# Kernel optimization log

Hardware: AMD Instinct MI355X
Metric: run time of the kernel (lower is better)

Reference implementation:

```python
import jax, jax.numpy as jnp
import numpy as np

N = 32768   # 'a' nodes
K = 8       # incoming edges per node (regular graph)
K2 = K // 2
E = N * K   # edges, stored as reverse pairs (2i, 2i+1)
D = 300     # hid_dim
H = 4       # attention heads
DEPTH = 3


def _build_graph():
    i = np.arange(N)
    src = np.empty(E, np.int64)
    mail = np.empty((N, K), np.int64)
    for d in range(1, K2 + 1):
        base = 2 * (i * K2 + (d - 1))
        src[base] = i                 # edge i -> (i+d)%N
        src[base + 1] = (i + d) % N   # reverse edge (i+d)%N -> i
        # incoming edges of node v: ((v-d)->v) and ((v+d)->v)
        mail[:, 2 * (d - 1)] = 2 * (((i - d) % N) * K2 + (d - 1))
        mail[:, 2 * (d - 1) + 1] = 2 * (i * K2 + (d - 1)) + 1
    return src, mail


def setup_inputs() -> dict:
    key = jax.random.key(0)
    ks = jax.random.split(key, 12)
    s = 1.0 / np.sqrt(D)
    src, mail = _build_graph()
    return {
        'f': jax.random.normal(ks[0], (N, D), jnp.float32),
        'x': jax.random.normal(ks[1], (E, D), jnp.float32),
        'mail_idx': jnp.asarray(mail),
        'src_idx': jnp.asarray(src),
        'Wq': jax.random.normal(ks[2], (D, D), jnp.float32) * s,
        'bq': jnp.zeros((D,), jnp.float32),
        'Wk': jax.random.normal(ks[3], (D, D), jnp.float32) * s,
        'bk': jnp.zeros((D,), jnp.float32),
        'Wv': jax.random.normal(ks[4], (D, D), jnp.float32) * s,
        'bv': jnp.zeros((D,), jnp.float32),
        'Wo': jax.random.normal(ks[5], (D, D), jnp.float32) * s,
        'bo': jnp.zeros((D,), jnp.float32),
        'Wmp': jax.random.normal(ks[6], (DEPTH - 1, D, D), jnp.float32) * s,
        'bmp': jnp.zeros((DEPTH - 1, D), jnp.float32),
        'Wlast': jax.random.normal(ks[7], (3 * D, D), jnp.float32) * s,
        'blast': jnp.zeros((D,), jnp.float32),
    }


def _mha(q_in, k_in, v_in, Wq, bq, Wk, bk, Wv, bv, Wo, bo):
    # q_in: [N,1,D], k_in/v_in: [N,K,D]  (per-node neighborhood attention)
    dk = D // H
    q = (q_in @ Wq + bq).reshape(N, 1, H, dk).transpose(0, 2, 1, 3)
    k = (k_in @ Wk + bk).reshape(N, -1, H, dk).transpose(0, 2, 1, 3)
    v = (v_in @ Wv + bv).reshape(N, -1, H, dk).transpose(0, 2, 1, 3)
    scores = jnp.einsum('nhqd,nhkd->nhqk', q, k) / jnp.sqrt(jnp.float32(dk))
    p = jax.nn.softmax(scores, axis=-1)
    o = jnp.einsum('nhqk,nhkd->nhqd', p, v).transpose(0, 2, 1, 3).reshape(N, 1, D)
    return o @ Wo + bo


def reference(f, x, mail_idx, src_idx, Wq, bq, Wk, bk, Wv, bv, Wo, bo,
              Wmp, bmp, Wlast, blast):
    rev = jnp.arange(E) ^ 1  # reverse_edge: swap within consecutive pairs
    f_h = f              # init_node: f_h = f.clone()
    h = x                # init_edge: h = x.clone()
    for i in range(DEPTH - 1):
        mail = h[mail_idx]                    # copy_e mailbox [N,K,D]
        feat = f_h[:, None, :]                # [N,1,D]
        # add_attn: attn(feat, mail, mail + feat)
        f_h = _mha(feat, mail, mail + feat,
                   Wq, bq, Wk, bk, Wv, bv, Wo, bo)[:, 0, :]
        rev_h = h[rev]                        # paired reverse-edge feature
        m = f_h[src_idx] - rev_h              # del_reverse_message
        h = jax.nn.relu(x + m @ Wmp[i] + bmp[i])  # update_edge
    # final node update: Linear(cat([sum(mailbox h), f_h, f]))
    mail_sum = jnp.sum(h[mail_idx], axis=1)   # [N,D]
    f_final = jnp.concatenate([mail_sum, f_h, f], axis=1) @ Wlast + blast
    return f_final
```

## Files before the change

kernel.cpp:

```cpp
#include <hip/hip_runtime.h>

typedef unsigned short u16;
typedef unsigned int u32;
typedef __bf16 bf16x8 __attribute__((ext_vector_type(8)));
typedef float f32x4 __attribute__((ext_vector_type(4)));

#define N_NODES 32768
#define E_EDGES 262144
#define BQ_U16 26240
#define S75 0.11547005383792515f

__device__ __forceinline__ float b2f(u16 u) {
    union { u32 u; float f; } x; x.u = ((u32)u) << 16; return x.f;
}
__device__ __forceinline__ u16 f2b(float f) {
    union { float f; u32 u; } x; x.f = f;
    u32 r = x.u + 0x7FFF + ((x.u >> 16) & 1);
    return (u16)(r >> 16);
}

#define GLOAD16(g, l) \
    __builtin_amdgcn_global_load_lds((const __attribute__((address_space(1))) u32*)(g), \
                                     (__attribute__((address_space(3))) u32*)(l), 16, 0, 0)

__global__ void convT_k(const float* __restrict__ src, int R, int C,
                        u16* __restrict__ dst, int KP_, long total) {
    long id = (long)blockIdx.x * blockDim.x + threadIdx.x;
    if (id >= total) return;
    int n = (int)(id / KP_), k = (int)(id % KP_);
    dst[id] = (k < R && n < C) ? f2b(src[(long)k * C + n]) : (u16)0;
}

__global__ void convTq_k(const float* __restrict__ src, u16* __restrict__ dst) {
    int id = blockIdx.x * 256 + threadIdx.x;
    if (id >= 4 * BQ_U16) return;
    int q = id / BQ_U16, rem = id % BQ_U16;
    int r = rem / 328, c = rem % 328;
    int n = q * 80 + r;
    dst[id] = (c < 300 && n < 300) ? f2b(src[(long)c * 300 + n]) : (u16)0;
}

__global__ void wqkq_k(const float* __restrict__ Wq, const float* __restrict__ Wk,
                       u16* __restrict__ dst) {
    int id = blockIdx.x * 256 + threadIdx.x;
    if (id >= 16 * BQ_U16) return;
    int q = id / BQ_U16, rem = id % BQ_U16;
    int r = rem / 328, c = rem % 328;
    int h = q >> 2;
    int cc = (q & 3) * 80 + r;
    float acc = 0.f;
    if (c < 300 && cc < 300) {
        const float* wq = Wq + (long)c * 300 + 75 * h;
        const float* wk = Wk + (long)cc * 300 + 75 * h;
        for (int d = 0; d < 75; ++d) acc += wq[d] * wk[d];
        acc *= S75;
    }
    dst[id] = f2b(acc);
}

__global__ void bqk_k(const float* __restrict__ bq, const float* __restrict__ Wk,
                      float* __restrict__ dst) {
    int n = blockIdx.x * 256 + threadIdx.x;
    if (n >= 1280) return;
    int h = n / 320, cc = n % 320;
    float acc = 0.f;
    if (cc < 300) {
        const float* b = bq + 75 * h;
        const float* wk = Wk + (long)cc * 300 + 75 * h;
        for (int d = 0; d < 75; ++d) acc += b[d] * wk[d];
        acc *= S75;
    }
    dst[n] = acc;
}

__global__ void ucatp_k(const float* __restrict__ Wv, const float* __restrict__ Wo,
                        u16* __restrict__ dst) {
    long id = (long)blockIdx.x * 256 + threadIdx.x;
    if (id >= 4L * 5 * BQ_U16) return;
    int q = (int)(id / (5 * BQ_U16));
    int rem = (int)(id % (5 * BQ_U16));
    int ph = rem / BQ_U16;
    int rem2 = rem % BQ_U16;
    int r = rem2 / 328, c = rem2 % 328;
    int n = q * 80 + r;
    float acc = 0.f;
    if (n < 300 && c < 320) {
        if (ph < 4) {
            int a = c;
            if (a < 300) {
                const float* wv = Wv + (long)a * 300 + 75 * ph;
                const float* wo = Wo + (long)(75 * ph) * 300 + n;
                for (int d = 0; d < 75; ++d) acc += wv[d] * wo[(long)d * 300];
            }
        } else {
            int a = c;
            if (a < 300) {
                const float* wv = Wv + (long)a * 300;
                const float* wo = Wo + n;
                for (int d = 0; d < 300; ++d) acc += wv[d] * wo[(long)d * 300];
            }
        }
    }
    dst[id] = f2b(acc);
}

__global__ void bvo_k(const float* __restrict__ bv, const float* __restrict__ Wo,
                      const float* __restrict__ bo, float* __restrict__ dst) {
    int n = blockIdx.x * 256 + threadIdx.x;
    if (n >= 320) return;
    float acc = 0.f;
    if (n < 300) {
        for (int d = 0; d < 300; ++d) acc += bv[d] * Wo[(long)d * 300 + n];
        acc += bo[n];
    }
    dst[n] = acc;
}

__global__ void padconv_k(const float* __restrict__ src, int C,
                          u16* __restrict__ dst, int CP,
                          u16* __restrict__ dst2, int CP2, long total) {
    long id = (long)blockIdx.x * blockDim.x + threadIdx.x;
    if (id >= total) return;
    int cw = CP >> 3;
    long row = id / cw;
    int c8 = (int)(id % cw) * 8;
    u32 w[4];
    #pragma unroll
    for (int p = 0; p < 4; ++p) {
        int c0 = c8 + 2 * p, c1 = c0 + 1;
        u16 lo = (c0 < C) ? f2b(src[row * C + c0]) : (u16)0;
        u16 hi = (c1 < C) ? f2b(src[row * C + c1]) : (u16)0;
        w[p] = (u32)lo | ((u32)hi << 16);
    }
    u32* d = (u32*)(dst + row * CP + c8);
    d[0] = w[0]; d[1] = w[1]; d[2] = w[2]; d[3] = w[3];
    if (dst2) {
        u32* d2 = (u32*)(dst2 + row * CP2 + c8);
        d2[0] = w[0]; d2[1] = w[1]; d2[2] = w[2]; d2[3] = w[3];
    }
}

__global__ void featcopy_k(const u16* __restrict__ src, u16* __restrict__ dst) {
    long id = (long)blockIdx.x * 256 + threadIdx.x;
    if (id >= (long)N_NODES * 40) return;
    long row = id / 40;
    int c8 = (int)(id % 40) * 8;
    *(uint4*)&dst[row * 1600 + 1280 + c8] = *(const uint4*)&src[row * 320 + c8];
}


#define GEMM16_SHARED \
    __shared__ __attribute__((aligned(16))) u16 Bs[3328 * 8];      \
    __shared__ __attribute__((aligned(16))) u16 dumpB[512];        \
    __shared__ __attribute__((aligned(16))) u16 As3[3][512 * 32];

#define GEMM16_PRE(QBITS, LDA) \
    const int tid = threadIdx.x; \
    const int w = tid >> 6, lane = tid & 63; \
    const int tl = lane & 15, thi = lane >> 4; \
    const int bid = blockIdx.x; \
    const int gid = (bid & 7) * ((int)gridDim.x >> 3) + (bid >> 3); \
    const long m0 = (long)(gid >> (QBITS)) * 512; \
    const int q = gid & ((1 << (QBITS)) - 1); \
    const int n0 = q * 80; \
    const int w_u = __builtin_amdgcn_readfirstlane(w); \
    const u16* Bsrc = Bswz + q * BQ_U16; \
     \
    _Pragma("unroll") \
    for (int i = 0; i < 3; ++i) \
        GLOAD16(Bsrc + (long)(i * 1024 + tid) * 8, &Bs[(i * 1024 + w_u * 64) * 8]); \
    { \
        int t = 3072 + tid; \
        int ts = t < 3280 ? t : 3279; \
        u16* bdst = (w_u < 4) ? &Bs[(3072 + w_u * 64) * 8] : dumpB; \
        GLOAD16(Bsrc + (long)ts * 8, bdst); \
    } \
    __builtin_amdgcn_sched_barrier(0); \
     \
    const int rr = lane >> 2;                  \
    const int gsrc = (lane & 3) ^ (rr & 3);    \
    const u16* pA0 = A + (m0 + w * 32 + rr) * (long)(LDA) + gsrc * 8; \
    const u16* pA1 = pA0 + 16L * (LDA); \
    u16* awbase = &As3[0][0];

#define ASTAGE16(KB) { \
    u16* d_ = &As3[(KB) % 3][w_u * 1024]; \
    GLOAD16(pA0 + (KB) * 32, d_); \
    GLOAD16(pA1 + (KB) * 32, d_ + 512); }

#define TCOMP16(KB) { \
    const u16* aw_ = &As3[(KB) % 3][w * 1024]; \
    bf16x8 a0_ = *(const bf16x8*)&aw_[tl * 32 + (thi ^ (tl & 3)) * 8]; \
    bf16x8 a1_ = *(const bf16x8*)&aw_[512 + tl * 32 + (thi ^ (tl & 3)) * 8]; \
    __builtin_amdgcn_s_setprio(1); \
    _Pragma("unroll") for (int fc = 0; fc < 5; ++fc) { \
        bf16x8 bb_ = *(const bf16x8*)&Bs[tl * 328 + thi * 8 + fc * 5248 + (KB) * 32]; \
        acc[0][fc] = __builtin_amdgcn_mfma_f32_16x16x32_bf16(bb_, a0_, acc[0][fc], 0, 0, 0); \
        acc[1][fc] = __builtin_amdgcn_mfma_f32_16x16x32_bf16(bb_, a1_, acc[1][fc], 0, 0, 0); } \
    __builtin_amdgcn_s_setprio(0); }

#define GEMM16_LOOP \
    ASTAGE16(0); ASTAGE16(1); ASTAGE16(2); \
    f32x4 acc[2][5]; \
    _Pragma("unroll") for (int i = 0; i < 2; ++i) \
        _Pragma("unroll") for (int j = 0; j < 5; ++j) acc[i][j] = (f32x4)(0.f); \
    asm volatile("s_waitcnt vmcnt(6)" ::: "memory");    \
    __builtin_amdgcn_s_barrier();                       \
    __builtin_amdgcn_sched_barrier(0); \
     \
    _Pragma("unroll") \
    for (int KB = 0; KB < 10; ++KB) { \
        if (KB <= 7)      { asm volatile("s_waitcnt vmcnt(4)" ::: "memory"); } \
        else if (KB == 8) { asm volatile("s_waitcnt vmcnt(2)" ::: "memory"); } \
        else              { asm volatile("s_waitcnt vmcnt(0)" ::: "memory"); } \
        __builtin_amdgcn_sched_barrier(0); \
        TCOMP16(KB); \
        asm volatile("s_waitcnt lgkmcnt(0)" ::: "memory");   \
        __builtin_amdgcn_sched_barrier(0); \
        if (KB + 3 < 10) ASTAGE16(KB + 3); \
    } \
    (void)awbase;

template<int QBITS, int OSTR>
__global__ __launch_bounds__(1024, 4) void ngemm16_k(
    const u16* __restrict__ A, const u16* __restrict__ Bswz,
    const float* __restrict__ bias, u16* __restrict__ outB)
{
    GEMM16_SHARED
    GEMM16_PRE(QBITS, 320)
    GEMM16_LOOP

    #pragma unroll
    for (int fr = 0; fr < 2; ++fr) {
        const long row = m0 + w * 32 + fr * 16 + tl;
        #pragma unroll
        for (int fc = 0; fc < 5; ++fc) {
            const int c0 = n0 + fc * 16 + thi * 4;
            f32x4 v = acc[fr][fc];
            if (bias) {
                const float4 bs = *(const float4*)&bias[c0];
                v[0] += bs.x; v[1] += bs.y; v[2] += bs.z; v[3] += bs.w;
            }
            uint2 p;
            p.x = (u32)f2b(v[0]) | ((u32)f2b(v[1]) << 16);
            p.y = (u32)f2b(v[2]) | ((u32)f2b(v[3]) << 16);
            *(uint2*)&outB[row * (long)OSTR + c0] = p;
        }
    }
}

__global__ __launch_bounds__(1024, 4) void hgemm16_k(
    const u16* __restrict__ A , const u16* __restrict__ Bswz ,
    const u16* __restrict__ FG, const u16* __restrict__ hx,
    const int* __restrict__ srcidx, const float* __restrict__ bias,
    u16* __restrict__ outB)
{
    GEMM16_SHARED
    GEMM16_PRE(2, 320)
    GEMM16_LOOP

    #pragma unroll
    for (int fr = 0; fr < 2; ++fr) {
        const long row = m0 + w * 32 + fr * 16 + tl;
        const int srow = srcidx[row];
        #pragma unroll
        for (int fc = 0; fc < 5; ++fc) {
            const int c0 = n0 + fc * 16 + thi * 4;
            float o0 = __shfl_xor(acc[fr][fc][0], 1, 64);
            float o1 = __shfl_xor(acc[fr][fc][1], 1, 64);
            float o2 = __shfl_xor(acc[fr][fc][2], 1, 64);
            float o3 = __shfl_xor(acc[fr][fc][3], 1, 64);
            const ushort4 fg = *(const ushort4*)&FG[(long)srow * 320 + c0];
            const ushort4 xv = *(const ushort4*)&hx[row * 320 + c0];
            float v0 = b2f(fg.x) + b2f(xv.x) - o0;
            float v1 = b2f(fg.y) + b2f(xv.y) - o1;
            float v2 = b2f(fg.z) + b2f(xv.z) - o2;
            float v3 = b2f(fg.w) + b2f(xv.w) - o3;
            if (c0 < 300) {
                const float4 bs = *(const float4*)&bias[c0];
                v0 += bs.x; v1 += bs.y; v2 += bs.z; v3 += bs.w;
            }
            v0 = fmaxf(v0, 0.f); v1 = fmaxf(v1, 0.f);
            v2 = fmaxf(v2, 0.f); v3 = fmaxf(v3, 0.f);
            uint2 p;
            p.x = (u32)f2b(v0) | ((u32)f2b(v1) << 16);
            p.y = (u32)f2b(v2) | ((u32)f2b(v3) << 16);
            *(uint2*)&outB[row * 320 + c0] = p;
        }
    }
}

#define TCOMP(KB, APTR) do { \
    bf16x8 av_[2], bb_[5]; \
    _Pragma("unroll") for (int fr = 0; fr < 2; ++fr) \
        av_[fr] = *(const bf16x8*)&(APTR)[ar0 + fr * 512]; \
    _Pragma("unroll") for (int fc = 0; fc < 5; ++fc) \
        bb_[fc] = *(const bf16x8*)&Bsw[br0 + fc * 5248 + (KB) * 32]; \
    __builtin_amdgcn_s_setprio(1); \
    _Pragma("unroll") for (int fr = 0; fr < 2; ++fr) \
        _Pragma("unroll") for (int fc = 0; fc < 5; ++fc) \
            acc[fr][fc] = __builtin_amdgcn_mfma_f32_16x16x32_bf16(bb_[fc], av_[fr], acc[fr][fc], 0, 0, 0); \
    __builtin_amdgcn_s_setprio(0); \
} while (0)

__global__ __launch_bounds__(256, 2) void wgemm_k(
    const u16* __restrict__ A , const u16* __restrict__ Bp,
    const float* __restrict__ bias, u16* __restrict__ outB)
{
    __shared__ __attribute__((aligned(16))) u16 Bsw[80 * 328];
    __shared__ __attribute__((aligned(16))) u16 As3[3][128 * 32];
    const int tid = threadIdx.x;
    const int wf = tid >> 6, lane = tid & 63;
    const int tl = lane & 15, thi = lane >> 4;
    const int bid = blockIdx.x;
    const int gid = (bid & 7) * ((int)gridDim.x >> 3) + (bid >> 3);
    const long m0 = (long)(gid >> 2) * 128;
    const int q = gid & 3;
    const int n0 = q * 80;
    const int wf_u = __builtin_amdgcn_readfirstlane(wf);
    const u16* BsrcQ = Bp + (long)q * (5 * BQ_U16);

    const int r1 = tid >> 2;
    const int g1 = (tid & 3) ^ ((r1 >> 1) & 3);
    const u16* gA0 = A + (m0 + r1) * 1600L + g1 * 8;
    const u16* gA1 = A + (m0 + 64 + r1) * 1600L + g1 * 8;

    f32x4 acc[2][5];
    #pragma unroll
    for (int i = 0; i < 2; ++i)
        #pragma unroll
        for (int j = 0; j < 5; ++j) acc[i][j] = (f32x4)(0.f);
    const int ar0 = (wf * 32 + tl) * 32 + (thi ^ ((tl >> 1) & 3)) * 8;
    const int br0 = tl * 328 + thi * 8;

    #pragma unroll
    for (int ph = 0; ph < 5; ++ph) {
        if (ph) __syncthreads();
        const u16* Bsrc = BsrcQ + ph * BQ_U16;
        #pragma unroll
        for (int i = 0; i < 13; ++i) {
            int t = i * 256 + tid;
            if (t < 3280)
                GLOAD16(Bsrc + (long)t * 8, &Bsw[(i * 256 + wf_u * 64) * 8]);
        }
        const long ko = (long)ph * 320;

#define WSTAGE(KB) { \
    GLOAD16(gA0 + ko + (KB) * 32, &As3[(KB) % 3][wf_u * 512]); \
    GLOAD16(gA1 + ko + (KB) * 32, &As3[(KB) % 3][2048 + wf_u * 512]); }

        WSTAGE(0); WSTAGE(1);

#define WSTEP(KB, VN) { \
    asm volatile("s_waitcnt vmcnt(" #VN ")" ::: "memory"); \
    __builtin_amdgcn_s_barrier(); \
    __builtin_amdgcn_sched_barrier(0); \
    if ((KB) + 2 < 10) WSTAGE((KB) + 2); \
    TCOMP(KB, (&As3[(KB) % 3][0])); }

        WSTEP(0, 2) WSTEP(1, 2) WSTEP(2, 2) WSTEP(3, 2) WSTEP(4, 2)
        WSTEP(5, 2) WSTEP(6, 2) WSTEP(7, 2) WSTEP(8, 2) WSTEP(9, 0)
#undef WSTEP
#undef WSTAGE
    }

    #pragma unroll
    for (int fr = 0; fr < 2; ++fr) {
        const long row = m0 + wf * 32 + fr * 16 + tl;
        #pragma unroll
        for (int fc = 0; fc < 5; ++fc) {
            const int c0 = n0 + fc * 16 + thi * 4;
            f32x4 v = acc[fr][fc];
            const float4 bs = *(const float4*)&bias[c0];
            v[0] += bs.x; v[1] += bs.y; v[2] += bs.z; v[3] += bs.w;
            uint2 p;
            p.x = (u32)f2b(v[0]) | ((u32)f2b(v[1]) << 16);
            p.y = (u32)f2b(v[2]) | ((u32)f2b(v[3]) << 16);
            *(uint2*)&outB[row * 320 + c0] = p;
        }
    }
}

__global__ __launch_bounds__(256) void attn2_k(
    const u16* __restrict__ qg, const u16* __restrict__ hcur,
    const int* __restrict__ mail, u16* __restrict__ wideA)
{
    const int tid = threadIdx.x;
    const long n = (long)blockIdx.x * 4 + (tid >> 6);
    const int lane = tid & 63;
    const bool act = lane < 40;
    const int ll = act ? lane : 39;

    int idx[8];
    #pragma unroll
    for (int j = 0; j < 8; ++j) idx[j] = mail[n * 8 + j];
    uint4 hr[8];
    #pragma unroll
    for (int j = 0; j < 8; ++j)
        hr[j] = *(const uint4*)&hcur[(long)idx[j] * 320 + ll * 8];
    uint4 qv[4];
    #pragma unroll
    for (int h = 0; h < 4; ++h)
        qv[h] = *(const uint4*)&qg[n * 1280 + h * 320 + ll * 8];
    if (!act) {
        #pragma unroll
        for (int j = 0; j < 8; ++j) hr[j] = make_uint4(0, 0, 0, 0);
    }

    float qf[4][8];
    #pragma unroll
    for (int h = 0; h < 4; ++h) {
        const u32 w[4] = {qv[h].x, qv[h].y, qv[h].z, qv[h].w};
        #pragma unroll
        for (int p = 0; p < 4; ++p) {
            qf[h][2 * p]     = b2f((u16)(w[p] & 0xFFFF));
            qf[h][2 * p + 1] = b2f((u16)(w[p] >> 16));
        }
    }

    float s[4][8];
    #pragma unroll
    for (int j = 0; j < 8; ++j) {
        float hf[8];
        const u32 w[4] = {hr[j].x, hr[j].y, hr[j].z, hr[j].w};
        #pragma unroll
        for (int p = 0; p < 4; ++p) {
            hf[2 * p]     = b2f((u16)(w[p] & 0xFFFF));
            hf[2 * p + 1] = b2f((u16)(w[p] >> 16));
        }
        #pragma unroll
        for (int h = 0; h < 4; ++h) {
            float d = 0.f;
            #pragma unroll
            for (int m = 0; m < 8; ++m) d += qf[h][m] * hf[m];
            d += __shfl_xor(d, 32, 64);
            d += __shfl_xor(d, 16, 64);
            d += __shfl_xor(d, 8, 64);
            d += __shfl_xor(d, 4, 64);
            d += __shfl_xor(d, 2, 64);
            d += __shfl_xor(d, 1, 64);
            s[h][j] = d;
        }
    }

    float p_[4][8];
    #pragma unroll
    for (int h = 0; h < 4; ++h) {
        float mx = s[h][0];
        #pragma unroll
        for (int j = 1; j < 8; ++j) mx = fmaxf(mx, s[h][j]);
        float sum = 0.f;
        #pragma unroll
        for (int j = 0; j < 8; ++j) { p_[h][j] = __expf(s[h][j] - mx); sum += p_[h][j]; }
        const float inv = 1.f / sum;
        #pragma unroll
        for (int j = 0; j < 8; ++j) p_[h][j] *= inv;
    }

    float y[4][8];
    #pragma unroll
    for (int h = 0; h < 4; ++h)
        #pragma unroll
        for (int m = 0; m < 8; ++m) y[h][m] = 0.f;
    #pragma unroll
    for (int j = 0; j < 8; ++j) {
        float hf[8];
        const u32 w[4] = {hr[j].x, hr[j].y, hr[j].z, hr[j].w};
        #pragma unroll
        for (int p = 0; p < 4; ++p) {
            hf[2 * p]     = b2f((u16)(w[p] & 0xFFFF));
            hf[2 * p + 1] = b2f((u16)(w[p] >> 16));
        }
        #pragma unroll
        for (int h = 0; h < 4; ++h)
            #pragma unroll
            for (int m = 0; m < 8; ++m) y[h][m] += p_[h][j] * hf[m];
    }
    if (act) {
        #pragma unroll
        for (int h = 0; h < 4; ++h) {
            uint4 o;
            o.x = (u32)f2b(y[h][0]) | ((u32)f2b(y[h][1]) << 16);
            o.y = (u32)f2b(y[h][2]) | ((u32)f2b(y[h][3]) << 16);
            o.z = (u32)f2b(y[h][4]) | ((u32)f2b(y[h][5]) << 16);
            o.w = (u32)f2b(y[h][6]) | ((u32)f2b(y[h][7]) << 16);
            *(uint4*)&wideA[n * 1600 + h * 320 + lane * 8] = o;
        }
    }
}

#define LOADB(bq, kt1) { const long ko_ = (long)(kt1) << 6; \
    _Pragma("unroll") for (int fc = 0; fc < 5; ++fc) \
      _Pragma("unroll") for (int ks = 0; ks < 2; ++ks) \
        bq[fc][ks] = *(const bf16x8*)(gBw + (long)fc * 16 * KP + ko_ + ks * 32); }

#define READA(lkt) { \
    _Pragma("unroll") for (int fr = 0; fr < 4; ++fr) \
      _Pragma("unroll") for (int ks = 0; ks < 2; ++ks) \
        a[fr][ks] = *(const bf16x8*)&As[(fr * 16 + tl) * 320 + ((((lkt) * 8 + ks * 4 + thi) ^ sx) * 8)]; }

#define DOMFMA(bq) { _Pragma("unroll") for (int fr = 0; fr < 4; ++fr) \
    _Pragma("unroll") for (int fc = 0; fc < 5; ++fc) \
      _Pragma("unroll") for (int ks = 0; ks < 2; ++ks) \
        acc[fr][fc] = __builtin_amdgcn_mfma_f32_16x16x32_bf16(bq[fc][ks], a[fr][ks], acc[fr][fc], 0, 0, 0); }

template<int KP>
__global__ __launch_bounds__(256, 2) void gemm_k(
    const u16* __restrict__ A,
    const u16* __restrict__ BT,
    const float* __restrict__ bias,
    float* __restrict__ outF, int ostride, int ocols)
{
    __shared__ u16 As[64 * 320];
    const int tid = threadIdx.x;
    const int w = tid >> 6, lane = tid & 63;
    const int tl = lane & 15, thi = lane >> 4;
    const int sx = tl & 7;
    const long m0 = (long)blockIdx.x * 64;
    const int w_u = __builtin_amdgcn_readfirstlane(w);

    const u16* gBw = BT + ((long)(w * 80 + tl)) * KP + thi * 8;

    f32x4 acc[4][5];
    #pragma unroll
    for (int i = 0; i < 4; ++i)
        #pragma unroll
        for (int j = 0; j < 5; ++j) acc[i][j] = (f32x4)(0.f);

    constexpr int NCH = KP / 320;
    constexpr int NST = KP >> 6;
    bf16x8 bA[5][2], bB[5][2], a[4][2];

    #pragma unroll
    for (int kb = 0; kb < NCH; ++kb) {
        if (kb) __syncthreads();
        #pragma unroll
        for (int i = 0; i < 10; ++i) {
            const int c = i * 256 + w_u * 64 + lane;
            const int r = c / 40, s = c - r * 40;
            GLOAD16(A + (m0 + r) * (long)KP + kb * 320 + ((s ^ (r & 7)) * 8),
                    &As[(i * 256 + w_u * 64) * 8]);
        }
        if (kb == 0) LOADB(bA, 0);
        __syncthreads();
        #pragma unroll
        for (int lkt = 0; lkt < 5; ++lkt) {
            const int kt = kb * 5 + lkt;
            if (kt + 1 < NST) {
                if (kt & 1) { LOADB(bA, kt + 1); } else { LOADB(bB, kt + 1); }
            }
            READA(lkt);
            if (kt & 1) { DOMFMA(bB); } else { DOMFMA(bA); }
        }
    }

    #pragma unroll
    for (int fr = 0; fr < 4; ++fr) {
        const long row = m0 + fr * 16 + tl;
        #pragma unroll
        for (int fc = 0; fc < 5; ++fc) {
            const int c0 = w * 80 + fc * 16 + thi * 4;
            f32x4 v = acc[fr][fc];
            if (bias && c0 < 300) {
                const float4 bs = *(const float4*)&bias[c0];
                v[0] += bs.x; v[1] += bs.y; v[2] += bs.z; v[3] += bs.w;
            }
            if (c0 < ocols)
                *(float4*)&outF[row * (long)ostride + c0] = make_float4(v[0], v[1], v[2], v[3]);
        }
    }
}

__global__ __launch_bounds__(256) void concat_k(
    const u16* __restrict__ hb, const u16* __restrict__ fhb,
    const float* __restrict__ f, const int* __restrict__ mail,
    u16* __restrict__ Acat)
{
    const long n = blockIdx.x;
    int m[8];
    #pragma unroll
    for (int j = 0; j < 8; ++j) m[j] = mail[n * 8 + j];
    for (int c = threadIdx.x; c < 960; c += 256) {
        float v;
        if (c < 300) {
            float s = 0.f;
            #pragma unroll
            for (int j = 0; j < 8; ++j) s += b2f(hb[(long)m[j] * 320 + c]);
            v = s;
        } else if (c < 600) v = b2f(fhb[n * 320 + (c - 300)]);
        else if (c < 900) v = f[n * 300 + (c - 600)];
        else v = 0.f;
        Acat[n * 960 + c] = f2b(v);
    }
}

extern "C" void kernel_launch(void* const* d_in, const int* in_sizes, int n_in,
                              void* d_out, int out_size, void* d_ws, size_t ws_size,
                              hipStream_t stream)
{
    const int N = N_NODES, E = E_EDGES;
    const float* f    = (const float*)d_in[0];
    const float* x    = (const float*)d_in[1];
    const int*   mail = (const int*)d_in[2];
    const int*   srcx = (const int*)d_in[3];
    const float* Wq = (const float*)d_in[4];   const float* bq = (const float*)d_in[5];
    const float* Wk = (const float*)d_in[6];
    const float* Wv = (const float*)d_in[8];   const float* bv = (const float*)d_in[9];
    const float* Wo = (const float*)d_in[10];  const float* bo = (const float*)d_in[11];
    const float* Wmp = (const float*)d_in[12]; const float* bmp = (const float*)d_in[13];
    const float* Wlast = (const float*)d_in[14]; const float* blast = (const float*)d_in[15];
    float* out = (float*)d_out;

    char* ws = (char*)d_ws;
    size_t off = 0;
    auto alloc = [&](size_t b) -> void* {
        void* p = ws + off; off += (b + 255) & ~(size_t)255; return p;
    };
    u16* hb    = (u16*)alloc((size_t)E * 320 * 2);
    u16* hb2   = (u16*)alloc((size_t)E * 320 * 2);
    u16* qgb   = (u16*)alloc((size_t)N * 1280 * 2);
    u16* wideA = (u16*)alloc((size_t)N * 1600 * 2);
    u16* fhb   = (u16*)alloc((size_t)N * 320 * 2);
    u16* FGb   = (u16*)alloc((size_t)N * 320 * 2);
    u16* Acat  = (u16*)alloc((size_t)N * 960 * 2);
    u16* WqkS  = (u16*)alloc((size_t)16 * BQ_U16 * 2);
    u16* Wm0S  = (u16*)alloc((size_t)4 * BQ_U16 * 2);
    u16* Wm1S  = (u16*)alloc((size_t)4 * BQ_U16 * 2);
    u16* UcatP = (u16*)alloc((size_t)4 * 5 * BQ_U16 * 2);
    u16* WcatB = (u16*)alloc((size_t)960 * 320 * 2);
    float* bqkF = (float*)alloc(1280 * 4);
    float* bvoF = (float*)alloc(320 * 4);

    {
        wqkq_k<<<(16 * BQ_U16 + 255) / 256, 256, 0, stream>>>(Wq, Wk, WqkS);
        bqk_k<<<5, 256, 0, stream>>>(bq, Wk, bqkF);
        ucatp_k<<<(int)((4L * 5 * BQ_U16 + 255) / 256), 256, 0, stream>>>(Wv, Wo, UcatP);
        bvo_k<<<2, 256, 0, stream>>>(bv, Wo, bo, bvoF);
        int blks = (4 * BQ_U16 + 255) / 256;
        convTq_k<<<blks, 256, 0, stream>>>(Wmp, Wm0S);
        convTq_k<<<blks, 256, 0, stream>>>(Wmp + 90000, Wm1S);
        long totc = (long)320 * 960;
        convT_k<<<(int)((totc + 255) / 256), 256, 0, stream>>>(Wlast, 900, 300, WcatB, 960, totc);
    }
    {
        long totE = (long)E * 40;
        padconv_k<<<(int)((totE + 255) / 256), 256, 0, stream>>>(x, 300, hb, 320, nullptr, 0, totE);
        long totN = (long)N * 40;
        padconv_k<<<(int)((totN + 255) / 256), 256, 0, stream>>>(f, 300, fhb, 320, wideA + 1280, 1600, totN);
    }

    const int GQG = (N / 512) * 16;
    const int GFG = (N / 512) * 4;
    const int GNW = (N / 128) * 4;
    const int GEH = (E / 512) * 4;

    for (int it = 0; it < 2; ++it) {
        const float* bmpi = bmp + it * 300;
        const u16* WmS = it ? Wm1S : Wm0S;
        const u16* hcur = it ? hb2 : hb;
        u16* hnxt = it ? hb : hb2;
        ngemm16_k<4, 1280><<<GQG, 1024, 0, stream>>>(fhb, WqkS, bqkF, qgb);
        attn2_k<<<N / 4, 256, 0, stream>>>(qgb, hcur, mail, wideA);
        wgemm_k<<<GNW, 256, 0, stream>>>(wideA, UcatP, bvoF, fhb);
        featcopy_k<<<(int)(((long)N * 40 + 255) / 256), 256, 0, stream>>>(fhb, wideA);
        ngemm16_k<2, 320><<<GFG, 1024, 0, stream>>>(fhb, WmS, nullptr, FGb);
        hgemm16_k<<<GEH, 1024, 0, stream>>>(hcur, WmS, FGb, hb, srcx, bmpi, hnxt);
    }

    concat_k<<<N, 256, 0, stream>>>(hb, fhb, f, mail, Acat);
    gemm_k<960><<<N / 64, 256, 0, stream>>>(Acat, WcatB, blast, out, 300, 300);
}
```

Measured before the change: 1.337 ms.

## Restructure bf16 GEMMs to keep A tile resident and loop over N-panels

Replaces the 1024-thread, 512-row GEMM kernels (one 80-column B panel per block, triple-buffered A streaming) with 512-thread kernels that load a 128-row A tile into LDS once and iterate over all output column panels, restaging B per panel. This cuts repeated reads of A across column panels and the grid-level panel decomposition. The cost is serialized B staging with __syncthreads and no overlap between B loads and compute. The bias is also pre-padded to 320 entries so the epilogue drops its bounds check.

```diff
diff --git a/kernel.cpp b/kernel.cpp
--- a/kernel.cpp
+++ b/kernel.cpp
@@ -116,6 +116,13 @@
     dst[n] = acc;
 }
 
+__global__ void padb_k(const float* __restrict__ bmp, float* __restrict__ dst) {
+    int id = blockIdx.x * 256 + threadIdx.x;
+    if (id >= 640) return;
+    int it = id / 320, c = id % 320;
+    dst[id] = (c < 300) ? bmp[it * 300 + c] : 0.f;
+}
+
 __global__ void padconv_k(const float* __restrict__ src, int C,
                           u16* __restrict__ dst, int CP,
                           u16* __restrict__ dst2, int CP2, long total) {
@@ -149,94 +156,73 @@
 }
 
 
-#define GEMM16_SHARED \
-    __shared__ __attribute__((aligned(16))) u16 Bs[3328 * 8];      \
-    __shared__ __attribute__((aligned(16))) u16 dumpB[512];        \
-    __shared__ __attribute__((aligned(16))) u16 As3[3][512 * 32];
-
-#define GEMM16_PRE(QBITS, LDA) \
+#define PG_SHARED \
+    __shared__ __attribute__((aligned(16))) u16 Al[128 * 328]; \
+    __shared__ __attribute__((aligned(16))) u16 Bs[80 * 328];
+
+#define PG_PRE \
     const int tid = threadIdx.x; \
     const int w = tid >> 6, lane = tid & 63; \
     const int tl = lane & 15, thi = lane >> 4; \
-    const int bid = blockIdx.x; \
-    const int gid = (bid & 7) * ((int)gridDim.x >> 3) + (bid >> 3); \
-    const long m0 = (long)(gid >> (QBITS)) * 512; \
-    const int q = gid & ((1 << (QBITS)) - 1); \
-    const int n0 = q * 80; \
+    const long m0 = (long)blockIdx.x * 128; \
     const int w_u = __builtin_amdgcn_readfirstlane(w); \
-    const u16* Bsrc = Bswz + q * BQ_U16; \
      \
     _Pragma("unroll") \
-    for (int i = 0; i < 3; ++i) \
-        GLOAD16(Bsrc + (long)(i * 1024 + tid) * 8, &Bs[(i * 1024 + w_u * 64) * 8]); \
-    { \
-        int t = 3072 + tid; \
-        int ts = t < 3280 ? t : 3279; \
-        u16* bdst = (w_u < 4) ? &Bs[(3072 + w_u * 64) * 8] : dumpB; \
-        GLOAD16(Bsrc + (long)ts * 8, bdst); \
+    for (int j = 0; j < 10; ++j) { \
+        int slot = j * 512 + tid; \
+        int r = slot / 41, s = slot % 41; \
+        GLOAD16(A + (m0 + r) * 320L + (s < 40 ? s : 39) * 8, \
+                &Al[(j * 512 + w_u * 64) * 8]); \
     } \
-    __builtin_amdgcn_sched_barrier(0); \
-     \
-    const int rr = lane >> 2;                  \
-    const int gsrc = (lane & 3) ^ (rr & 3);    \
-    const u16* pA0 = A + (m0 + w * 32 + rr) * (long)(LDA) + gsrc * 8; \
-    const u16* pA1 = pA0 + 16L * (LDA); \
-    u16* awbase = &As3[0][0];
-
-#define ASTAGE16(KB) { \
-    u16* d_ = &As3[(KB) % 3][w_u * 1024]; \
-    GLOAD16(pA0 + (KB) * 32, d_); \
-    GLOAD16(pA1 + (KB) * 32, d_ + 512); }
-
-#define TCOMP16(KB) { \
-    const u16* aw_ = &As3[(KB) % 3][w * 1024]; \
-    bf16x8 a0_ = *(const bf16x8*)&aw_[tl * 32 + (thi ^ (tl & 3)) * 8]; \
-    bf16x8 a1_ = *(const bf16x8*)&aw_[512 + tl * 32 + (thi ^ (tl & 3)) * 8]; \
-    __builtin_amdgcn_s_setprio(1); \
-    _Pragma("unroll") for (int fc = 0; fc < 5; ++fc) { \
-        bf16x8 bb_ = *(const bf16x8*)&Bs[tl * 328 + thi * 8 + fc * 5248 + (KB) * 32]; \
-        acc[0][fc] = __builtin_amdgcn_mfma_f32_16x16x32_bf16(bb_, a0_, acc[0][fc], 0, 0, 0); \
-        acc[1][fc] = __builtin_amdgcn_mfma_f32_16x16x32_bf16(bb_, a1_, acc[1][fc], 0, 0, 0); } \
-    __builtin_amdgcn_s_setprio(0); }
-
-#define GEMM16_LOOP \
-    ASTAGE16(0); ASTAGE16(1); ASTAGE16(2); \
-    f32x4 acc[2][5]; \
-    _Pragma("unroll") for (int i = 0; i < 2; ++i) \
-        _Pragma("unroll") for (int j = 0; j < 5; ++j) acc[i][j] = (f32x4)(0.f); \
-    asm volatile("s_waitcnt vmcnt(6)" ::: "memory");    \
-    __builtin_amdgcn_s_barrier();                       \
-    __builtin_amdgcn_sched_barrier(0); \
-     \
+    if (tid < 128) { \
+        int slot = 5120 + tid; \
+        int r = slot / 41, s = slot % 41; \
+        GLOAD16(A + (m0 + r) * 320L + (s < 40 ? s : 39) * 8, \
+                &Al[(5120 + w_u * 64) * 8]); \
+    }
+
+#define PG_STAGEB(QQ) { \
+    const u16* Bsrc_ = Bq + (QQ) * BQ_U16; \
+    _Pragma("unroll") \
+    for (int j = 0; j < 7; ++j) { \
+        int t = j * 512 + tid; \
+        if (t < 3280) \
+            GLOAD16(Bsrc_ + (long)t * 8, &Bs[(j * 512 + w_u * 64) * 8]); \
+    } }
+
+#define PG_COMPUTE \
+    f32x4 acc[5]; \
+    _Pragma("unroll") for (int fc = 0; fc < 5; ++fc) acc[fc] = (f32x4)(0.f); \
     _Pragma("unroll") \
     for (int KB = 0; KB < 10; ++KB) { \
-        if (KB <= 7)      { asm volatile("s_waitcnt vmcnt(4)" ::: "memory"); } \
-        else if (KB == 8) { asm volatile("s_waitcnt vmcnt(2)" ::: "memory"); } \
-        else              { asm volatile("s_waitcnt vmcnt(0)" ::: "memory"); } \
-        __builtin_amdgcn_sched_barrier(0); \
-        TCOMP16(KB); \
-        asm volatile("s_waitcnt lgkmcnt(0)" ::: "memory");   \
-        __builtin_amdgcn_sched_barrier(0); \
-        if (KB + 3 < 10) ASTAGE16(KB + 3); \
-    } \
-    (void)awbase;
-
-template<int QBITS, int OSTR>
-__global__ __launch_bounds__(1024, 4) void ngemm16_k(
-    const u16* __restrict__ A, const u16* __restrict__ Bswz,
+        bf16x8 a_ = *(const bf16x8*)&Al[(w * 16 + tl) * 328 + thi * 8 + KB * 32]; \
+        __builtin_amdgcn_s_setprio(1); \
+        _Pragma("unroll") for (int fc = 0; fc < 5; ++fc) { \
+            bf16x8 bb_ = *(const bf16x8*)&Bs[(fc * 16 + tl) * 328 + thi * 8 + KB * 32]; \
+            acc[fc] = __builtin_amdgcn_mfma_f32_16x16x32_bf16(bb_, a_, acc[fc], 0, 0, 0); \
+        } \
+        __builtin_amdgcn_s_setprio(0); \
+    }
+
+template<int NPH, int OSTR>
+__global__ __launch_bounds__(512, 2) void pgemm_k(
+    const u16* __restrict__ A, const u16* __restrict__ Bq,
     const float* __restrict__ bias, u16* __restrict__ outB)
 {
-    GEMM16_SHARED
-    GEMM16_PRE(QBITS, 320)
-    GEMM16_LOOP
-
-    #pragma unroll
-    for (int fr = 0; fr < 2; ++fr) {
-        const long row = m0 + w * 32 + fr * 16 + tl;
+    PG_SHARED
+    PG_PRE
+    PG_STAGEB(0)
+    const long row = m0 + w * 16 + tl;
+
+    for (int q = 0; q < NPH; ++q) {
+        __syncthreads();
+        PG_COMPUTE
+        __syncthreads();
+        if (q + 1 < NPH) PG_STAGEB(q + 1)
         #pragma unroll
         for (int fc = 0; fc < 5; ++fc) {
-            const int c0 = n0 + fc * 16 + thi * 4;
-            f32x4 v = acc[fr][fc];
+            const int c0 = q * 80 + fc * 16 + thi * 4;
+            f32x4 v = acc[fc];
             if (bias) {
                 const float4 bs = *(const float4*)&bias[c0];
                 v[0] += bs.x; v[1] += bs.y; v[2] += bs.z; v[3] += bs.w;
@@ -249,37 +235,37 @@
     }
 }
 
-__global__ __launch_bounds__(1024, 4) void hgemm16_k(
-    const u16* __restrict__ A , const u16* __restrict__ Bswz ,
+__global__ __launch_bounds__(512, 2) void phgemm_k(
+    const u16* __restrict__ A , const u16* __restrict__ Bq ,
     const u16* __restrict__ FG, const u16* __restrict__ hx,
-    const int* __restrict__ srcidx, const float* __restrict__ bias,
+    const int* __restrict__ srcidx, const float* __restrict__ bias ,
     u16* __restrict__ outB)
 {
-    GEMM16_SHARED
-    GEMM16_PRE(2, 320)
-    GEMM16_LOOP
-
-    #pragma unroll
-    for (int fr = 0; fr < 2; ++fr) {
-        const long row = m0 + w * 32 + fr * 16 + tl;
-        const int srow = srcidx[row];
+    PG_SHARED
+    PG_PRE
+    PG_STAGEB(0)
+    const long row = m0 + w * 16 + tl;
+    const int srow = srcidx[row];
+
+    for (int q = 0; q < 4; ++q) {
+        __syncthreads();
+        PG_COMPUTE
+        __syncthreads();
+        if (q + 1 < 4) PG_STAGEB(q + 1)
         #pragma unroll
         for (int fc = 0; fc < 5; ++fc) {
-            const int c0 = n0 + fc * 16 + thi * 4;
-            float o0 = __shfl_xor(acc[fr][fc][0], 1, 64);
-            float o1 = __shfl_xor(acc[fr][fc][1], 1, 64);
-            float o2 = __shfl_xor(acc[fr][fc][2], 1, 64);
-            float o3 = __shfl_xor(acc[fr][fc][3], 1, 64);
+            const int c0 = q * 80 + fc * 16 + thi * 4;
+            float o0 = __shfl_xor(acc[fc][0], 1, 64);
+            float o1 = __shfl_xor(acc[fc][1], 1, 64);
+            float o2 = __shfl_xor(acc[fc][2], 1, 64);
+            float o3 = __shfl_xor(acc[fc][3], 1, 64);
             const ushort4 fg = *(const ushort4*)&FG[(long)srow * 320 + c0];
             const ushort4 xv = *(const ushort4*)&hx[row * 320 + c0];
-            float v0 = b2f(fg.x) + b2f(xv.x) - o0;
-            float v1 = b2f(fg.y) + b2f(xv.y) - o1;
-            float v2 = b2f(fg.z) + b2f(xv.z) - o2;
-            float v3 = b2f(fg.w) + b2f(xv.w) - o3;
-            if (c0 < 300) {
-                const float4 bs = *(const float4*)&bias[c0];
-                v0 += bs.x; v1 += bs.y; v2 += bs.z; v3 += bs.w;
-            }
+            const float4 bs = *(const float4*)&bias[c0];
+            float v0 = b2f(fg.x) + b2f(xv.x) - o0 + bs.x;
+            float v1 = b2f(fg.y) + b2f(xv.y) - o1 + bs.y;
+            float v2 = b2f(fg.z) + b2f(xv.z) - o2 + bs.z;
+            float v3 = b2f(fg.w) + b2f(xv.w) - o3 + bs.w;
             v0 = fmaxf(v0, 0.f); v1 = fmaxf(v1, 0.f);
             v2 = fmaxf(v2, 0.f); v3 = fmaxf(v3, 0.f);
             uint2 p;
@@ -630,12 +616,14 @@
     u16* WcatB = (u16*)alloc((size_t)960 * 320 * 2);
     float* bqkF = (float*)alloc(1280 * 4);
     float* bvoF = (float*)alloc(320 * 4);
+    float* bmpP = (float*)alloc(640 * 4);
 
     {
         wqkq_k<<<(16 * BQ_U16 + 255) / 256, 256, 0, stream>>>(Wq, Wk, WqkS);
         bqk_k<<<5, 256, 0, stream>>>(bq, Wk, bqkF);
         ucatp_k<<<(int)((4L * 5 * BQ_U16 + 255) / 256), 256, 0, stream>>>(Wv, Wo, UcatP);
         bvo_k<<<2, 256, 0, stream>>>(bv, Wo, bo, bvoF);
+        padb_k<<<3, 256, 0, stream>>>(bmp, bmpP);
         int blks = (4 * BQ_U16 + 255) / 256;
         convTq_k<<<blks, 256, 0, stream>>>(Wmp, Wm0S);
         convTq_k<<<blks, 256, 0, stream>>>(Wmp + 90000, Wm1S);
@@ -649,22 +637,20 @@
         padconv_k<<<(int)((totN + 255) / 256), 256, 0, stream>>>(f, 300, fhb, 320, wideA + 1280, 1600, totN);
     }
 
-    const int GQG = (N / 512) * 16;
-    const int GFG = (N / 512) * 4;
+    const int GN = N / 128;
+    const int GE = E / 128;
     const int GNW = (N / 128) * 4;
-    const int GEH = (E / 512) * 4;
 
     for (int it = 0; it < 2; ++it) {
-        const float* bmpi = bmp + it * 300;
         const u16* WmS = it ? Wm1S : Wm0S;
         const u16* hcur = it ? hb2 : hb;
         u16* hnxt = it ? hb : hb2;
-        ngemm16_k<4, 1280><<<GQG, 1024, 0, stream>>>(fhb, WqkS, bqkF, qgb);
+        pgemm_k<16, 1280><<<GN, 512, 0, stream>>>(fhb, WqkS, bqkF, qgb);
         attn2_k<<<N / 4, 256, 0, stream>>>(qgb, hcur, mail, wideA);
         wgemm_k<<<GNW, 256, 0, stream>>>(wideA, UcatP, bvoF, fhb);
         featcopy_k<<<(int)(((long)N * 40 + 255) / 256), 256, 0, stream>>>(fhb, wideA);
-        ngemm16_k<2, 320><<<GFG, 1024, 0, stream>>>(fhb, WmS, nullptr, FGb);
-        hgemm16_k<<<GEH, 1024, 0, stream>>>(hcur, WmS, FGb, hb, srcx, bmpi, hnxt);
+        pgemm_k<4, 320><<<GN, 512, 0, stream>>>(fhb, WmS, nullptr, FGb);
+        phgemm_k<<<GE, 512, 0, stream>>>(hcur, WmS, FGb, hb, srcx, bmpP + it * 320, hnxt);
     }
 
     concat_k<<<N, 256, 0, stream>>>(hb, fhb, f, mail, Acat);
```

New measurement: 1.409 ms. 5.4% more time.
